# Performance work log

Measured on AMD Instinct MI355X. Metric: run time of the kernel, lower is better.

Reference implementation:

```python
import jax, jax.numpy as jnp
import numpy as np


def _gcn_conv(x, src, dst, norm, W, b, n_nodes):
    # PyG GCNConv: transform then normalized scatter-add aggregation.
    h = x @ W                                        # [N, F_out]
    msg = h[src] * norm[:, None]                     # [E+N, F_out] gather
    out = jax.ops.segment_sum(msg, dst, num_segments=n_nodes)  # scatter-add
    return out + b


def setup_inputs() -> dict:
    key = jax.random.key(0)
    ks = jax.random.split(key, 8)
    N, E, F_in, H, C = 100000, 1000000, 128, 64, 40
    x = jax.random.normal(ks[0], (N, F_in), dtype=jnp.float32)
    edge_index = jax.random.randint(ks[1], (2, E), 0, N, dtype=jnp.int64)
    W1 = jax.random.normal(ks[2], (F_in, H), dtype=jnp.float32) * (1.0 / np.sqrt(F_in))
    b1 = jnp.zeros((H,), jnp.float32)
    W2 = jax.random.normal(ks[3], (H, H), dtype=jnp.float32) * (1.0 / np.sqrt(H))
    b2 = jnp.zeros((H,), jnp.float32)
    Wc = jax.random.normal(ks[4], (H, C), dtype=jnp.float32) * (1.0 / np.sqrt(H))
    bc = jnp.zeros((C,), jnp.float32)
    return {"x": x, "edge_index": edge_index, "W1": W1, "b1": b1,
            "W2": W2, "b2": b2, "Wc": Wc, "bc": bc}


def reference(x, edge_index, W1, b1, W2, b2, Wc, bc):
    n_nodes = x.shape[0]
    # Add self loops (GCNConv default), symmetric normalization.
    loop = jnp.arange(n_nodes, dtype=edge_index.dtype)
    src = jnp.concatenate([edge_index[0], loop])
    dst = jnp.concatenate([edge_index[1], loop])
    deg = jax.ops.segment_sum(jnp.ones_like(dst, jnp.float32), dst,
                              num_segments=n_nodes)
    dinv = jnp.where(deg > 0, jax.lax.rsqrt(jnp.maximum(deg, 1.0)), 0.0)
    norm = dinv[src] * dinv[dst]                     # [E+N]

    h = jax.nn.relu(_gcn_conv(x, src, dst, norm, W1, b1, n_nodes))
    # dropout: identity (inference / training=False)
    h = jax.nn.relu(_gcn_conv(h, src, dst, norm, W2, b2, n_nodes))
    return h @ Wc + bc                               # [N, out_dim]
```

## Files before the change

kernel.cpp:

```cpp
#include <hip/hip_runtime.h>
#include <hip/hip_fp16.h>


#define BUCKET_BITS  8
#define BUCKET_NODES 256
#define MAXB 512
#define CAP  8192
#define OFF_MASK 0x3FFFFF

typedef _Float16 half8 __attribute__((ext_vector_type(8)));
typedef float    f32x4 __attribute__((ext_vector_type(4)));

union H8  { uint4 u; __half h[8]; };
union HV8 { uint4 u; half8 h; };

__global__ void zero_kernel(int* __restrict__ p, int n) {
    int i = blockIdx.x * blockDim.x + threadIdx.x;
    if (i < n) p[i] = 0;
}

__global__ __launch_bounds__(256) void bucket_fill_kernel(const int* __restrict__ src,
                                                          const int* __restrict__ dst,
                                                          int* __restrict__ bucketCursor,
                                                          unsigned int* __restrict__ bucketArr,
                                                          int E, int NB) {
    __shared__ int lcnt[MAXB];
    for (int i = threadIdx.x; i < NB; i += 256) lcnt[i] = 0;
    __syncthreads();
    const int base = blockIdx.x * 2048;
    int d[8], s[8];
#pragma unroll
    for (int k = 0; k < 8; ++k) {
        int e = base + k * 256 + threadIdx.x;
        bool ok = e < E;
        d[k] = ok ? dst[e] : -1;
        s[k] = ok ? src[e] : 0;
    }
#pragma unroll
    for (int k = 0; k < 8; ++k)
        if (d[k] >= 0) atomicAdd(&lcnt[d[k] >> BUCKET_BITS], 1);
    __syncthreads();
    for (int i = threadIdx.x; i < NB; i += 256) {
        int c = lcnt[i];
        if (c) lcnt[i] = i * CAP + atomicAdd(&bucketCursor[i], c);
    }
    __syncthreads();
#pragma unroll
    for (int k = 0; k < 8; ++k)
        if (d[k] >= 0) {
            int pos = atomicAdd(&lcnt[d[k] >> BUCKET_BITS], 1);
            bucketArr[pos] = ((unsigned)(d[k] & (BUCKET_NODES - 1)) << 24) | (unsigned)s[k];
        }
}

__global__ __launch_bounds__(1024) void node_sort_kernel(const unsigned int* __restrict__ bucketArr,
                                                         const int* __restrict__ bucketCursor,
                                                         unsigned int* __restrict__ nodeInfo,
                                                         float* __restrict__ dinv,
                                                         unsigned int* __restrict__ adj, int N) {
    __shared__ int cnt[BUCKET_NODES];
    __shared__ int scn[BUCKET_NODES];
    __shared__ int cur[BUCKET_NODES];
    const int t = threadIdx.x;
    const int b = blockIdx.x;
    if (t < BUCKET_NODES) cnt[t] = 0;
    __syncthreads();
    const int e0 = b * CAP;
    const int e1 = e0 + bucketCursor[b];
    for (int e = e0 + t; e < e1; e += 1024)
        atomicAdd(&cnt[bucketArr[e] >> 24], 1);
    __syncthreads();
    if (t < BUCKET_NODES) scn[t] = cnt[t];
    __syncthreads();
    for (int off = 1; off < BUCKET_NODES; off <<= 1) {
        int u = 0;
        if (t < BUCKET_NODES && t >= off) u = scn[t - off];
        __syncthreads();
        if (t < BUCKET_NODES) scn[t] += u;
        __syncthreads();
    }
    if (t < BUCKET_NODES) {
        const int v    = cnt[t];
        const int excl = scn[t] - v;
        const int node = b * BUCKET_NODES + t;
        if (node < N) {
            nodeInfo[node] = ((unsigned)v << 22) | (unsigned)(e0 + excl);
            dinv[node]     = rsqrtf((float)(v + 1));
        }
        cur[t] = e0 + excl;
    }
    __syncthreads();
    for (int e = e0 + t; e < e1; e += 1024) {
        unsigned int entry = bucketArr[e];
        int pos = atomicAdd(&cur[entry >> 24], 1);
        adj[pos] = entry & 0xFFFFFF;
    }
}

template <int K, int NOUT, int NCT, bool AHALF, bool OHALF, bool SCALE, bool BIAS>
__global__ __launch_bounds__(256) void gemm_mfma(const void* __restrict__ Av,
                                                 const float* __restrict__ W,
                                                 const float* __restrict__ bias,
                                                 const float* __restrict__ dscale,
                                                 void* __restrict__ outv, int M) {
    constexpr int KP = K + 8;
    __shared__ _Float16 WTh[64 * KP];
    __shared__ _Float16 WTl[64 * KP];

    for (int i = threadIdx.x; i < K * 64; i += 256) {
        int k = i >> 6, c = i & 63;
        float w = (NOUT == 64 || c < NOUT) ? W[k * NOUT + c] : 0.f;
        _Float16 h = (_Float16)w;
        WTh[c * KP + k] = h;
        WTl[c * KP + k] = (_Float16)(w - (float)h);
    }
    __syncthreads();

    const int lane = threadIdx.x & 63;
    const int wv   = threadIdx.x >> 6;
    const int r    = lane & 15;
    const int q    = lane >> 4;
    int arow = blockIdx.x * 64 + wv * 16 + r;
    if (arow > M - 1) arow = M - 1;

    f32x4 acc[NCT] = {};

#pragma unroll
    for (int kst = 0; kst < K; kst += 32) {
        half8 ah = {}, al = {};
        if (AHALF) {
            HV8 v;
            v.u = *(const uint4*)((const __half*)Av + (size_t)arow * K + kst + q * 8);
            ah = v.h;
        } else {
            const float* ap = (const float*)Av + (size_t)arow * K + kst + q * 8;
            float4 f0 = *(const float4*)ap;
            float4 f1 = *(const float4*)(ap + 4);
            float fs[8] = {f0.x, f0.y, f0.z, f0.w, f1.x, f1.y, f1.z, f1.w};
#pragma unroll
            for (int j = 0; j < 8; ++j) {
                _Float16 h = (_Float16)fs[j];
                ah[j] = h;
                al[j] = (_Float16)(fs[j] - (float)h);
            }
        }
#pragma unroll
        for (int n = 0; n < NCT; ++n) {
            const int bo = (n * 16 + r) * KP + kst + q * 8;
            HV8 bh, bl;
            bh.u = *(const uint4*)(WTh + bo);
            bl.u = *(const uint4*)(WTl + bo);
            acc[n] = __builtin_amdgcn_mfma_f32_16x16x32_f16(ah, bh.h, acc[n], 0, 0, 0);
            acc[n] = __builtin_amdgcn_mfma_f32_16x16x32_f16(ah, bl.h, acc[n], 0, 0, 0);
            if (!AHALF)
                acc[n] = __builtin_amdgcn_mfma_f32_16x16x32_f16(al, bh.h, acc[n], 0, 0, 0);
        }
    }

    const int orow0 = blockIdx.x * 64 + wv * 16 + q * 4;
#pragma unroll
    for (int n = 0; n < NCT; ++n) {
        const int col = n * 16 + r;
        float bb = 0.f;
        if (BIAS) bb = (col < NOUT) ? bias[col] : 0.f;
#pragma unroll
        for (int j = 0; j < 4; ++j) {
            const int row = orow0 + j;
            if (row >= M) break;
            const float sc = SCALE ? dscale[row] : 1.f;
            const float v = acc[n][j] * sc + bb;
            if (OHALF) {
                ((__half*)outv)[(size_t)row * NOUT + col] = __float2half(v);
            } else if (col < NOUT) {
                ((float*)outv)[(size_t)row * NOUT + col] = v;
            }
        }
    }
}

__global__ __launch_bounds__(256) void gather_kernel(const __half* __restrict__ h,
                                                     const unsigned int* __restrict__ nodeInfo,
                                                     const unsigned int* __restrict__ adj,
                                                     const float* __restrict__ dinv,
                                                     const float* __restrict__ bias,
                                                     __half* __restrict__ out, int N) {
    const int node = blockIdx.x * 32 + (threadIdx.x >> 3);
    const int l    = threadIdx.x & 7;
    if (node >= N) return;

    const unsigned info = nodeInfo[node];
    const int start = (int)(info & OFF_MASK);
    const int end   = start + (int)(info >> 22);
    const float di  = dinv[node];

    float acc[8];
    {
        H8 sv;
        sv.u = *(const uint4*)(h + (size_t)node * 64 + l * 8);
#pragma unroll
        for (int k = 0; k < 8; ++k) acc[k] = __half2float(sv.h[k]);
    }

    for (int base = start; ; base += 8) {
        bool active = base < end;
        if (__ballot(active) == 0ull) break;
        const int m = active ? min(8, end - base) : 0;

        int s[8];
#pragma unroll
        for (int j = 0; j < 8; ++j) s[j] = (int)adj[base + j];

        uint4 rv[8];
#pragma unroll
        for (int j = 0; j < 8; ++j)
            if (j < m) rv[j] = *(const uint4*)(h + (size_t)s[j] * 64 + l * 8);

#pragma unroll
        for (int j = 0; j < 8; ++j)
            if (j < m) {
                H8 t;
                t.u = rv[j];
#pragma unroll
                for (int k = 0; k < 8; ++k) acc[k] += __half2float(t.h[k]);
            }
    }

    const float4 b0 = *(const float4*)(bias + l * 8);
    const float4 b1 = *(const float4*)(bias + l * 8 + 4);
    const float bb[8] = {b0.x, b0.y, b0.z, b0.w, b1.x, b1.y, b1.z, b1.w};
    H8 ov;
#pragma unroll
    for (int k = 0; k < 8; ++k) {
        float v = acc[k] * di + bb[k];
        ov.h[k] = __float2half(v > 0.f ? v : 0.f);
    }
    *(uint4*)(out + (size_t)node * 64 + l * 8) = ov.u;
}

extern "C" void kernel_launch(void* const* d_in, const int* in_sizes, int n_in,
                              void* d_out, int out_size, void* d_ws, size_t ws_size,
                              hipStream_t stream) {
    const float* x  = (const float*)d_in[0];
    const int*   ei = (const int*)d_in[1];
    const float* W1 = (const float*)d_in[2];
    const float* b1 = (const float*)d_in[3];
    const float* W2 = (const float*)d_in[4];
    const float* b2 = (const float*)d_in[5];
    const float* Wc = (const float*)d_in[6];
    const float* bc = (const float*)d_in[7];

    const int N = in_sizes[0] / 128;
    const int E = in_sizes[1] / 2;
    const int* src = ei;
    const int* dst = ei + E;

    const int NB = (N + BUCKET_NODES - 1) >> BUCKET_BITS;
    const int EB = (E + 2047) / 2048;

    char* w = (char*)d_ws;
    auto alloc = [&](size_t bytes) { char* p = w; w += (bytes + 255) & ~(size_t)255; return p; };
    int*          bucketCursor = (int*)alloc((size_t)NB * 4);
    unsigned int* bucketArr    = (unsigned int*)alloc((size_t)NB * CAP * 4);
    unsigned int* nodeInfo     = (unsigned int*)alloc((size_t)N * 4);
    unsigned int* adj          = (unsigned int*)alloc((size_t)NB * CAP * 4);
    float*        dinv         = (float*)alloc((size_t)N * 4);
    __half*       bufA         = (__half*)alloc((size_t)N * 64 * 2);
    __half*       bufB         = (__half*)alloc((size_t)N * 64 * 2);

    dim3 blk(256);
    const int nblkG = (N + 63) / 64;
    const int nblkV = (N + 31) / 32;

    zero_kernel<<<(NB + 255) / 256, blk, 0, stream>>>(bucketCursor, NB);
    bucket_fill_kernel<<<EB, blk, 0, stream>>>(src, dst, bucketCursor, bucketArr, E, NB);
    node_sort_kernel<<<NB, dim3(1024), 0, stream>>>(bucketArr, bucketCursor, nodeInfo, dinv, adj, N);

    gemm_mfma<128, 64, 4, false, true, true, false><<<nblkG, blk, 0, stream>>>(
        x, W1, nullptr, dinv, bufA, N);
    gather_kernel<<<nblkV, blk, 0, stream>>>(bufA, nodeInfo, adj, dinv, b1, bufB, N);

    gemm_mfma<64, 64, 4, true, true, true, false><<<nblkG, blk, 0, stream>>>(
        bufB, W2, nullptr, dinv, bufA, N);
    gather_kernel<<<nblkV, blk, 0, stream>>>(bufA, nodeInfo, adj, dinv, b2, bufB, N);

    gemm_mfma<64, 40, 3, true, false, false, true><<<nblkG, blk, 0, stream>>>(
        bufB, Wc, bc, nullptr, d_out, N);
}
```

Baseline: 219.4 us.

## Stage bucket fill and node sort through shared memory for coalesced writes

The bucket-fill kernel now handles 8192-edge chunks per 512-thread block. It sorts entries locally in LDS by bucket, then writes them out contiguously using a binary search over the prefix-scanned bucket offsets. This is meant to turn scattered global writes into coalesced runs and to reduce global atomics on the bucket cursors. The node-sort kernel caches its bucket window in LDS, so it reads global memory once instead of twice. In exchange, chunks are larger and there are fewer blocks, each with heavy LDS use, plus a per-element binary search.

```diff
diff --git a/kernel.cpp b/kernel.cpp
--- a/kernel.cpp
+++ b/kernel.cpp
@@ -7,6 +7,7 @@
 #define MAXB 512
 #define CAP  8192
 #define OFF_MASK 0x3FFFFF
+#define CHUNK 8192
 
 typedef _Float16 half8 __attribute__((ext_vector_type(8)));
 typedef float    f32x4 __attribute__((ext_vector_type(4)));
@@ -19,45 +20,70 @@
     if (i < n) p[i] = 0;
 }
 
-__global__ __launch_bounds__(256) void bucket_fill_kernel(const int* __restrict__ src,
+__global__ __launch_bounds__(512) void bucket_fill_kernel(const int* __restrict__ src,
                                                           const int* __restrict__ dst,
                                                           int* __restrict__ bucketCursor,
                                                           unsigned int* __restrict__ bucketArr,
                                                           int E, int NB) {
-    __shared__ int lcnt[MAXB];
-    for (int i = threadIdx.x; i < NB; i += 256) lcnt[i] = 0;
-    __syncthreads();
-    const int base = blockIdx.x * 2048;
-    int d[8], s[8];
-#pragma unroll
-    for (int k = 0; k < 8; ++k) {
-        int e = base + k * 256 + threadIdx.x;
-        bool ok = e < E;
-        d[k] = ok ? dst[e] : -1;
-        s[k] = ok ? src[e] : 0;
-    }
-#pragma unroll
-    for (int k = 0; k < 8; ++k)
-        if (d[k] >= 0) atomicAdd(&lcnt[d[k] >> BUCKET_BITS], 1);
-    __syncthreads();
-    for (int i = threadIdx.x; i < NB; i += 256) {
-        int c = lcnt[i];
-        if (c) lcnt[i] = i * CAP + atomicAdd(&bucketCursor[i], c);
-    }
-    __syncthreads();
-#pragma unroll
-    for (int k = 0; k < 8; ++k)
-        if (d[k] >= 0) {
-            int pos = atomicAdd(&lcnt[d[k] >> BUCKET_BITS], 1);
-            bucketArr[pos] = ((unsigned)(d[k] & (BUCKET_NODES - 1)) << 24) | (unsigned)s[k];
-        }
-}
-
-__global__ __launch_bounds__(1024) void node_sort_kernel(const unsigned int* __restrict__ bucketArr,
-                                                         const int* __restrict__ bucketCursor,
-                                                         unsigned int* __restrict__ nodeInfo,
-                                                         float* __restrict__ dinv,
-                                                         unsigned int* __restrict__ adj, int N) {
+    __shared__ unsigned int ent[CHUNK];
+    __shared__ int scn[MAXB];
+    __shared__ int lcur[MAXB];
+    __shared__ int gofs[MAXB];
+    const int t = threadIdx.x;
+    lcur[t] = 0;
+    __syncthreads();
+
+    const int base  = blockIdx.x * CHUNK;
+    const int count = min(CHUNK, E - base);
+
+    for (int i = t; i < count; i += 512)
+        atomicAdd(&lcur[dst[base + i] >> BUCKET_BITS], 1);
+    __syncthreads();
+
+    scn[t] = lcur[t];
+    __syncthreads();
+    for (int off = 1; off < MAXB; off <<= 1) {
+        int a = (t >= off) ? scn[t - off] : 0;
+        __syncthreads();
+        scn[t] += a;
+        __syncthreads();
+    }
+
+    {
+        const int c  = lcur[t];
+        const int lo = scn[t] - c;
+        int g = 0;
+        if (c > 0 && t < NB) g = t * CAP + atomicAdd(&bucketCursor[t], c);
+        gofs[t] = g - lo;
+        lcur[t] = lo;
+    }
+    __syncthreads();
+
+    for (int i = t; i < count; i += 512) {
+        const int d = dst[base + i];
+        const int s = src[base + i];
+        const int b = d >> BUCKET_BITS;
+        const int p = atomicAdd(&lcur[b], 1);
+        ent[p] = ((unsigned)(d & (BUCKET_NODES - 1)) << 24) | (unsigned)s;
+    }
+    __syncthreads();
+
+    for (int j = t; j < count; j += 512) {
+        int lo2 = 0, hi2 = MAXB - 1;
+        while (lo2 < hi2) {
+            int mid = (lo2 + hi2) >> 1;
+            if (scn[mid] > j) hi2 = mid; else lo2 = mid + 1;
+        }
+        bucketArr[gofs[lo2] + j] = ent[j];
+    }
+}
+
+__global__ __launch_bounds__(512) void node_sort_kernel(const unsigned int* __restrict__ bucketArr,
+                                                        const int* __restrict__ bucketCursor,
+                                                        unsigned int* __restrict__ nodeInfo,
+                                                        float* __restrict__ dinv,
+                                                        unsigned int* __restrict__ adj, int N) {
+    __shared__ unsigned int win[CAP];
     __shared__ int cnt[BUCKET_NODES];
     __shared__ int scn[BUCKET_NODES];
     __shared__ int cur[BUCKET_NODES];
@@ -65,18 +91,24 @@
     const int b = blockIdx.x;
     if (t < BUCKET_NODES) cnt[t] = 0;
     __syncthreads();
+
     const int e0 = b * CAP;
-    const int e1 = e0 + bucketCursor[b];
-    for (int e = e0 + t; e < e1; e += 1024)
-        atomicAdd(&cnt[bucketArr[e] >> 24], 1);
-    __syncthreads();
+    const int total = bucketCursor[b];
+
+    for (int i = t; i < total; i += 512) {
+        const unsigned e = bucketArr[e0 + i];
+        win[i] = e;
+        atomicAdd(&cnt[e >> 24], 1);
+    }
+    __syncthreads();
+
     if (t < BUCKET_NODES) scn[t] = cnt[t];
     __syncthreads();
     for (int off = 1; off < BUCKET_NODES; off <<= 1) {
-        int u = 0;
-        if (t < BUCKET_NODES && t >= off) u = scn[t - off];
+        int a = 0;
+        if (t < BUCKET_NODES && t >= off) a = scn[t - off];
         __syncthreads();
-        if (t < BUCKET_NODES) scn[t] += u;
+        if (t < BUCKET_NODES) scn[t] += a;
         __syncthreads();
     }
     if (t < BUCKET_NODES) {
@@ -87,13 +119,14 @@
             nodeInfo[node] = ((unsigned)v << 22) | (unsigned)(e0 + excl);
             dinv[node]     = rsqrtf((float)(v + 1));
         }
-        cur[t] = e0 + excl;
-    }
-    __syncthreads();
-    for (int e = e0 + t; e < e1; e += 1024) {
-        unsigned int entry = bucketArr[e];
-        int pos = atomicAdd(&cur[entry >> 24], 1);
-        adj[pos] = entry & 0xFFFFFF;
+        cur[t] = excl;
+    }
+    __syncthreads();
+
+    for (int i = t; i < total; i += 512) {
+        const unsigned entry = win[i];
+        const int p = atomicAdd(&cur[entry >> 24], 1);
+        adj[e0 + p] = entry & 0xFFFFFF;
     }
 }
 
@@ -218,10 +251,10 @@
 #pragma unroll
         for (int j = 0; j < 8; ++j)
             if (j < m) {
-                H8 t;
-                t.u = rv[j];
-#pragma unroll
-                for (int k = 0; k < 8; ++k) acc[k] += __half2float(t.h[k]);
+                H8 tt;
+                tt.u = rv[j];
+#pragma unroll
+                for (int k = 0; k < 8; ++k) acc[k] += __half2float(tt.h[k]);
             }
     }
 
@@ -255,7 +288,7 @@
     const int* dst = ei + E;
 
     const int NB = (N + BUCKET_NODES - 1) >> BUCKET_BITS;
-    const int EB = (E + 2047) / 2048;
+    const int EB = (E + CHUNK - 1) / CHUNK;
 
     char* w = (char*)d_ws;
     auto alloc = [&](size_t bytes) { char* p = w; w += (bytes + 255) & ~(size_t)255; return p; };
@@ -272,8 +305,8 @@
     const int nblkV = (N + 31) / 32;
 
     zero_kernel<<<(NB + 255) / 256, blk, 0, stream>>>(bucketCursor, NB);
-    bucket_fill_kernel<<<EB, blk, 0, stream>>>(src, dst, bucketCursor, bucketArr, E, NB);
-    node_sort_kernel<<<NB, dim3(1024), 0, stream>>>(bucketArr, bucketCursor, nodeInfo, dinv, adj, N);
+    bucket_fill_kernel<<<EB, dim3(512), 0, stream>>>(src, dst, bucketCursor, bucketArr, E, NB);
+    node_sort_kernel<<<NB, dim3(512), 0, stream>>>(bucketArr, bucketCursor, nodeInfo, dinv, adj, N);
 
     gemm_mfma<128, 64, 4, false, true, true, false><<<nblkG, blk, 0, stream>>>(
         x, W1, nullptr, dinv, bufA, N);
```

After: 223.0 us. About the same (+1.6%).
